# Performance work log

Measured on AMD Instinct MI355X. Metric: run time of the kernel, lower is better.

The kernel has to match this reference:

```python
import jax, jax.numpy as jnp
import numpy as np

CODEBOOK_DIM = 12          # log2(codebook_size)
CODEBOOK_SIZE = 4096
DIM = 512
INV_TEMPERATURE = 100.0
CODEBOOK_SCALE = 1.0
DIVERSITY_GAMMA = 1.0
ENTROPY_LOSS_WEIGHT = 0.1
EPS = 1e-5


def setup_inputs() -> dict:
    key = jax.random.key(0)
    k_x, k_wi, k_wo = jax.random.split(key, 3)
    x = jax.random.normal(k_x, (4, 4096, DIM), dtype=jnp.float32)
    # nn.Linear weights: (out_features, in_features)
    w_in = jax.random.normal(k_wi, (CODEBOOK_DIM, DIM), dtype=jnp.float32) * 0.02
    b_in = jnp.zeros((CODEBOOK_DIM,), dtype=jnp.float32)
    w_out = jax.random.normal(k_wo, (DIM, CODEBOOK_DIM), dtype=jnp.float32) * 0.02
    b_out = jnp.zeros((DIM,), dtype=jnp.float32)
    return {"x": x, "w_in": w_in, "b_in": b_in, "w_out": w_out, "b_out": b_out}


def _entropy(prob):
    return (-prob * jnp.log(jnp.clip(prob, EPS))).sum(axis=-1)


def _make_codebook():
    mask = (2 ** jnp.arange(CODEBOOK_DIM - 1, -1, -1)).astype(jnp.int32)  # [d]
    all_codes = jnp.arange(CODEBOOK_SIZE, dtype=jnp.int32)
    bits = ((all_codes[:, None] & mask) != 0).astype(jnp.float32)  # [cs, d]
    codebook = bits * CODEBOOK_SCALE * 2 - CODEBOOK_SCALE  # {-1, +1}
    return mask, codebook


def reference(x, w_in, b_in, w_out, b_out):
    mask, codebook = _make_codebook()

    # project in: [b, n, dim] -> [b, n, d]
    xp = jnp.einsum('bnd,cd->bnc', x, w_in) + b_in  # c == codebook_dim here

    # sign quantization (num_codebooks = 1, so c-dim is implicit)
    quantized = jnp.where(xp > 0, CODEBOOK_SCALE, -CODEBOOK_SCALE).astype(xp.dtype)
    indices = ((quantized > 0).astype(jnp.int32) * mask).sum(axis=-1)  # [b, n]

    # straight-through estimator (training path)
    x_st = xp + jax.lax.stop_gradient(quantized - xp)

    # entropy aux loss over full codebook (frac_per_sample_entropy = 1.0)
    flat = xp.reshape(-1, CODEBOOK_DIM)  # original (pre-quant) input, [bn, d]
    # -distance * inv_temp = 2 * inv_temp * <x, code>
    logits = (2.0 * INV_TEMPERATURE) * (flat @ codebook.T)  # [bn, cs]
    prob = jax.nn.softmax(logits, axis=-1)
    per_sample_entropy = _entropy(prob).mean()
    avg_prob = prob.mean(axis=0)  # [cs]
    codebook_entropy = _entropy(avg_prob)
    entropy_aux_loss = per_sample_entropy - DIVERSITY_GAMMA * codebook_entropy
    aux_loss = entropy_aux_loss * ENTROPY_LOSS_WEIGHT

    # project out: [b, n, d] -> [b, n, dim]
    out = jnp.einsum('bnc,dc->bnd', x_st, w_out) + b_out
    return out, indices, aux_loss
```

## Files before the change

kernel.cpp:

```cpp
#include <hip/hip_runtime.h>
#include <hip/hip_bf16.h>


#define NS    16384
#define NOUT  (NS*512)
#define AUXO  (NOUT+NS)
#define INVT2 200.0f
#define NBLK  512

__global__ __launch_bounds__(512) void k_table(const float* __restrict__ w_out,
                                               const float* __restrict__ b_out,
                                               float* __restrict__ T) {
  __shared__ float s_wt[6144];
  const int t = threadIdx.x;
  #pragma unroll
  for (int k = 0; k < 12; ++k) s_wt[t + k * 512] = w_out[t * 12 + k];
  __syncthreads();

  const int c = blockIdx.x * 16 + (t >> 5);
  float sg[12];
  #pragma unroll
  for (int d = 0; d < 12; ++d) sg[d] = ((c >> (11 - d)) & 1) ? 1.f : -1.f;

  float4* Trow = (float4*)(T + (size_t)c * 512);
  #pragma unroll
  for (int k4 = 0; k4 < 4; ++k4) {
    const int m = (t & 31) + k4 * 32;
    float4 bo = ((const float4*)b_out)[m];
    float4 o = bo;
    #pragma unroll
    for (int d = 0; d < 12; ++d) {
      float4 w4 = ((const float4*)s_wt)[d * 128 + m];
      o.x += sg[d] * w4.x; o.y += sg[d] * w4.y; o.z += sg[d] * w4.z; o.w += sg[d] * w4.w;
    }
    Trow[m] = o;
  }
}

__global__ __launch_bounds__(512, 4) void k_main(
    const float* __restrict__ x,
    const float* __restrict__ w_in,  const float* __restrict__ b_in,
    const float* __restrict__ T,
    float* __restrict__ out, float* __restrict__ idx_out,
    float* __restrict__ P, float* __restrict__ Csum) {

  __shared__ float s_wi[6144];
  __shared__ float s_phi[32][64];
  __shared__ float s_psi[32][64];
  __shared__ float s_xp[8][4][12];
  __shared__ float s_h[8];

  const int t = threadIdx.x;

  #pragma unroll
  for (int k = 0; k < 12; ++k) {
    int f  = t + k * 512;
    int kk = f & 3;
    int q  = f >> 2;
    int sub = q & 15, e4 = (q >> 4) & 7, d = q >> 7;
    int e  = sub * 32 + e4 * 4 + kk;
    s_wi[f] = w_in[d * 512 + e];
  }
  __syncthreads();

  const int wave = t >> 6, lane = t & 63;
  const int g = lane >> 4, sub = lane & 15;

  float bin[12];
  #pragma unroll
  for (int d = 0; d < 12; ++d) bin[d] = b_in[d];

  const int i0 = blockIdx.x * 32 + wave * 4 + g;

  const float4* xr0 = (const float4*)(x + (size_t)i0 * 512 + sub * 32);
  float4 xv0[8];
  #pragma unroll
  for (int e4 = 0; e4 < 8; ++e4) xv0[e4] = xr0[e4];

  float p0[12];
  #pragma unroll
  for (int d = 0; d < 12; ++d) p0[d] = 0.f;
  #pragma unroll
  for (int e4 = 0; e4 < 8; ++e4) {
    #pragma unroll
    for (int d = 0; d < 12; ++d) {
      float4 w4 = ((const float4*)s_wi)[d * 128 + e4 * 16 + sub];
      p0[d] += xv0[e4].x * w4.x + xv0[e4].y * w4.y + xv0[e4].z * w4.z + xv0[e4].w * w4.w;
    }
  }
  #pragma unroll
  for (int d = 0; d < 12; ++d) {
    #pragma unroll
    for (int m = 1; m <= 8; m <<= 1) {
      p0[d] += __shfl_xor(p0[d], m, 16);
    }
    p0[d] += bin[d];
  }

  unsigned idx0 = 0u;
  #pragma unroll
  for (int d = 0; d < 12; ++d) {
    idx0 |= (p0[d] > 0.f ? 1u : 0u) << (11 - d);
  }
  if (sub == 0) {
    idx_out[i0] = (float)idx0;
    #pragma unroll
    for (int d = 0; d < 12; ++d) s_xp[wave][g][d] = p0[d];
  }

  {
    const float4* Trow = (const float4*)(T + (size_t)idx0 * 512);
    float4* or0 = (float4*)(out + (size_t)i0 * 512);
    #pragma unroll
    for (int e4 = 0; e4 < 8; ++e4) {
      or0[e4 * 16 + sub] = Trow[e4 * 16 + sub];
    }
  }

  float hacc = 0.f;
  #pragma unroll 1
  for (int s = 0; s < 4; ++s) {
    float xq[12];
    #pragma unroll
    for (int d = 0; d < 12; ++d) xq[d] = s_xp[wave][s][d];

    float hi = 0.f, lo = 0.f, ah = 0.f, al = 0.f;
    #pragma unroll
    for (int d = 0; d < 6; ++d) {
      int bh = (lane >> (5 - d)) & 1;
      hi += bh ? xq[d]     : -xq[d];
      lo += bh ? xq[6 + d] : -xq[6 + d];
      ah += fabsf(xq[d]);
      al += fabsf(xq[6 + d]);
    }
    float lhi = INVT2 * (hi - ah);
    float llo = INVT2 * (lo - al);
    float ehi = __expf(lhi);
    float elo = __expf(llo);
    float Shi = ehi, Slo = elo;
    #pragma unroll
    for (int m = 1; m <= 32; m <<= 1) {
      Shi += __shfl_xor(Shi, m);
      Slo += __shfl_xor(Slo, m);
    }
    float phi = ehi / Shi;
    float psi = elo / Slo;
    float lnShi = __logf(Shi), lnSlo = __logf(Slo);
    hacc += phi * (lhi - lnShi) + psi * (llo - lnSlo);

    const int ws = wave * 4 + s;
    s_phi[ws][lane] = phi;
    s_psi[ws][lane] = psi;
  }

  #pragma unroll
  for (int m = 1; m <= 32; m <<= 1) hacc += __shfl_xor(hacc, m);
  if (lane == 0) s_h[wave] = hacc;
  __syncthreads();
  if (t == 0) {
    float hs = 0.f;
    for (int w2 = 0; w2 < 8; ++w2) hs += s_h[w2];
    atomicAdd(Csum, hs);
  }

  const int jb = (t >> 5) * 4;
  const int lb = (t & 31) * 2;
  float a00 = 0.f, a01 = 0.f, a10 = 0.f, a11 = 0.f;
  float a20 = 0.f, a21 = 0.f, a30 = 0.f, a31 = 0.f;
  #pragma unroll 4
  for (int s = 0; s < 32; ++s) {
    float4 ph = *(const float4*)&s_phi[s][jb];
    float2 ps = *(const float2*)&s_psi[s][lb];
    a00 += ph.x * ps.x; a01 += ph.x * ps.y;
    a10 += ph.y * ps.x; a11 += ph.y * ps.y;
    a20 += ph.z * ps.x; a21 += ph.z * ps.y;
    a30 += ph.w * ps.x; a31 += ph.w * ps.y;
  }
  float* Pr = P + (size_t)blockIdx.x * 4096;
  *(float2*)&Pr[(jb + 0) * 64 + lb] = make_float2(a00, a01);
  *(float2*)&Pr[(jb + 1) * 64 + lb] = make_float2(a10, a11);
  *(float2*)&Pr[(jb + 2) * 64 + lb] = make_float2(a20, a21);
  *(float2*)&Pr[(jb + 3) * 64 + lb] = make_float2(a30, a31);
}

__global__ __launch_bounds__(256) void k_reduce(const float* __restrict__ P,
                                                float* __restrict__ scal,
                                                float* __restrict__ aux) {
  __shared__ float red[16][17];
  __shared__ float ered[16];
  const int t = threadIdx.x;
  const int cl = t & 15, rg = t >> 4;
  const int c = blockIdx.x * 16 + cl;
  float s = 0.f;
  #pragma unroll
  for (int k = 0; k < 32; ++k) s += P[(size_t)(rg + k * 16) * 4096 + c];
  red[rg][cl] = s;
  __syncthreads();
  if (t < 16) {
    float tot = 0.f;
    #pragma unroll
    for (int r = 0; r < 16; ++r) tot += red[r][t];
    float pb = tot * (1.f / (float)NS);
    ered[t] = pb * __logf(fmaxf(pb, 1e-5f));
  }
  __syncthreads();
  if (t == 0) {
    float e = 0.f;
    #pragma unroll
    for (int r = 0; r < 16; ++r) e += ered[r];
    atomicAdd(&scal[1], e);
    __threadfence();
    unsigned done = atomicAdd((unsigned*)&scal[2], 1u);
    if (done == 255u) {
      float E = atomicAdd(&scal[1], 0.f);
      float C = atomicAdd(&scal[0], 0.f);
      float per_sample_entropy = -C * (1.f / (float)NS);
      float codebook_entropy   = -E;
      aux[0] = 0.1f * (per_sample_entropy - codebook_entropy);
    }
  }
}

extern "C" void kernel_launch(void* const* d_in, const int* in_sizes, int n_in,
                              void* d_out, int out_size, void* d_ws, size_t ws_size,
                              hipStream_t stream) {
  const float* x     = (const float*)d_in[0];
  const float* w_in  = (const float*)d_in[1];
  const float* b_in  = (const float*)d_in[2];
  const float* w_out = (const float*)d_in[3];
  const float* b_out = (const float*)d_in[4];
  float* out = (float*)d_out;

  float* T    = (float*)d_ws;
  float* P    = T + (size_t)4096 * 512;
  float* scal = P + (size_t)NBLK * 4096;

  hipMemsetAsync(scal, 0, 3 * sizeof(float), stream);
  k_table<<<256, 512, 0, stream>>>(w_out, b_out, T);
  k_main<<<NBLK, 512, 0, stream>>>(x, w_in, b_in, T,
                                   out, out + NOUT, P, scal);
  k_reduce<<<256, 256, 0, stream>>>(P, scal, out + AUXO);
}
```

Before: 120.2 us.

## Use DPP/readlane wave reductions in k_main and restructure k_reduce into fewer blocks

In k_main, the per-sample projected vectors are broadcast across the wave with readlane instead of being staged in shared memory, and the 64-lane softmax sums use DPP row ops plus readlane instead of shfl_xor. The s-loop is fully unrolled. k_reduce now runs 64 blocks that each handle 64 contiguous columns with 4 row groups, which gives coalesced reads and a shuffle-based entropy sum. The aim is to cut LDS traffic, shuffle latency and reduce-kernel overhead. The risks are fewer blocks for the reduction, so less parallelism over the 8 MB partial buffer, and higher register pressure from the unrolled loop.

```diff
diff --git a/kernel.cpp b/kernel.cpp
--- a/kernel.cpp
+++ b/kernel.cpp
@@ -7,6 +7,16 @@
 #define AUXO  (NOUT+NS)
 #define INVT2 200.0f
 #define NBLK  512
+#define RBLK  64
+
+template <int CTRL>
+__device__ inline float dpp_add(float v) {
+  int p = __builtin_amdgcn_update_dpp(0, __float_as_int(v), CTRL, 0xF, 0xF, true);
+  return v + __int_as_float(p);
+}
+__device__ inline float rdlane(float v, int lane) {
+  return __int_as_float(__builtin_amdgcn_readlane(__float_as_int(v), lane));
+}
 
 __global__ __launch_bounds__(512) void k_table(const float* __restrict__ w_out,
                                                const float* __restrict__ b_out,
@@ -47,7 +57,6 @@
   __shared__ float s_wi[6144];
   __shared__ float s_phi[32][64];
   __shared__ float s_psi[32][64];
-  __shared__ float s_xp[8][4][12];
   __shared__ float s_h[8];
 
   const int t = threadIdx.x;
@@ -104,8 +113,6 @@
   }
   if (sub == 0) {
     idx_out[i0] = (float)idx0;
-    #pragma unroll
-    for (int d = 0; d < 12; ++d) s_xp[wave][g][d] = p0[d];
   }
 
   {
@@ -118,11 +125,11 @@
   }
 
   float hacc = 0.f;
-  #pragma unroll 1
+  #pragma unroll
   for (int s = 0; s < 4; ++s) {
     float xq[12];
     #pragma unroll
-    for (int d = 0; d < 12; ++d) xq[d] = s_xp[wave][s][d];
+    for (int d = 0; d < 12; ++d) xq[d] = rdlane(p0[d], 16 * s);
 
     float hi = 0.f, lo = 0.f, ah = 0.f, al = 0.f;
     #pragma unroll
@@ -137,12 +144,19 @@
     float llo = INVT2 * (lo - al);
     float ehi = __expf(lhi);
     float elo = __expf(llo);
+
     float Shi = ehi, Slo = elo;
-    #pragma unroll
-    for (int m = 1; m <= 32; m <<= 1) {
-      Shi += __shfl_xor(Shi, m);
-      Slo += __shfl_xor(Slo, m);
-    }
+    Shi = dpp_add<0xB1>(Shi);  Slo = dpp_add<0xB1>(Slo);
+    Shi = dpp_add<0x4E>(Shi);  Slo = dpp_add<0x4E>(Slo);
+    Shi = dpp_add<0x141>(Shi); Slo = dpp_add<0x141>(Slo);
+    Shi = dpp_add<0x140>(Shi); Slo = dpp_add<0x140>(Slo);
+    {
+      float r0 = rdlane(Shi, 0), r1 = rdlane(Shi, 16), r2 = rdlane(Shi, 32), r3 = rdlane(Shi, 48);
+      Shi = (r0 + r1) + (r2 + r3);
+      float q0 = rdlane(Slo, 0), q1 = rdlane(Slo, 16), q2 = rdlane(Slo, 32), q3 = rdlane(Slo, 48);
+      Slo = (q0 + q1) + (q2 + q3);
+    }
+
     float phi = ehi / Shi;
     float psi = elo / Slo;
     float lnShi = __logf(Shi), lnSlo = __logf(Slo);
@@ -186,37 +200,32 @@
 __global__ __launch_bounds__(256) void k_reduce(const float* __restrict__ P,
                                                 float* __restrict__ scal,
                                                 float* __restrict__ aux) {
-  __shared__ float red[16][17];
-  __shared__ float ered[16];
+  __shared__ float red[4][64];
   const int t = threadIdx.x;
-  const int cl = t & 15, rg = t >> 4;
-  const int c = blockIdx.x * 16 + cl;
+  const int c = blockIdx.x * 64 + (t & 63);
+  const int rg = t >> 6;
   float s = 0.f;
-  #pragma unroll
-  for (int k = 0; k < 32; ++k) s += P[(size_t)(rg + k * 16) * 4096 + c];
-  red[rg][cl] = s;
-  __syncthreads();
-  if (t < 16) {
-    float tot = 0.f;
-    #pragma unroll
-    for (int r = 0; r < 16; ++r) tot += red[r][t];
+  #pragma unroll 8
+  for (int j = 0; j < 128; ++j) s += P[(size_t)(rg * 128 + j) * 4096 + c];
+  red[rg][t & 63] = s;
+  __syncthreads();
+  if (t < 64) {
+    float tot = (red[0][t] + red[1][t]) + (red[2][t] + red[3][t]);
     float pb = tot * (1.f / (float)NS);
-    ered[t] = pb * __logf(fmaxf(pb, 1e-5f));
-  }
-  __syncthreads();
-  if (t == 0) {
-    float e = 0.f;
-    #pragma unroll
-    for (int r = 0; r < 16; ++r) e += ered[r];
-    atomicAdd(&scal[1], e);
-    __threadfence();
-    unsigned done = atomicAdd((unsigned*)&scal[2], 1u);
-    if (done == 255u) {
-      float E = atomicAdd(&scal[1], 0.f);
-      float C = atomicAdd(&scal[0], 0.f);
-      float per_sample_entropy = -C * (1.f / (float)NS);
-      float codebook_entropy   = -E;
-      aux[0] = 0.1f * (per_sample_entropy - codebook_entropy);
+    float e = pb * __logf(fmaxf(pb, 1e-5f));
+    #pragma unroll
+    for (int m = 1; m <= 32; m <<= 1) e += __shfl_xor(e, m);
+    if (t == 0) {
+      atomicAdd(&scal[1], e);
+      __threadfence();
+      unsigned done = atomicAdd((unsigned*)&scal[2], 1u);
+      if (done == RBLK - 1) {
+        float E = atomicAdd(&scal[1], 0.f);
+        float C = atomicAdd(&scal[0], 0.f);
+        float per_sample_entropy = -C * (1.f / (float)NS);
+        float codebook_entropy   = -E;
+        aux[0] = 0.1f * (per_sample_entropy - codebook_entropy);
+      }
     }
   }
 }
@@ -239,5 +248,5 @@
   k_table<<<256, 512, 0, stream>>>(w_out, b_out, T);
   k_main<<<NBLK, 512, 0, stream>>>(x, w_in, b_in, T,
                                    out, out + NOUT, P, scal);
-  k_reduce<<<256, 256, 0, stream>>>(P, scal, out + AUXO);
-}
+  k_reduce<<<RBLK, 256, 0, stream>>>(P, scal, out + AUXO);
+}
```

After: 118.9 us. No clear change (-1.0%).
